# Optimization experiments

Measured on AMD Instinct MI355X. Metric: run time of the kernel, lower is better.

The kernel has to match this reference:

```python
import jax, jax.numpy as jnp
import numpy as np


def _skew(p):
    # (..., 3) -> (..., 3, 3) skew-symmetric matrices
    x, y, z = p[..., 0], p[..., 1], p[..., 2]
    o = jnp.zeros_like(x)
    return jnp.stack([
        jnp.stack([o, -z, y], -1),
        jnp.stack([z, o, -x], -1),
        jnp.stack([-y, x, o], -1)], -2)


def _so3exp(w):
    # Rodrigues formula for a single (3,) axis-angle vector
    th2 = jnp.sum(w * w)
    th = jnp.sqrt(th2 + 1e-24)
    W = _skew(w)
    I = jnp.eye(3, dtype=w.dtype)
    A = jnp.sin(th) / th
    B = (1.0 - jnp.cos(th)) / (th2 + 1e-24)
    return I + A * W + B * (W @ W)


def _gather(fmap, ys, xs):
    # fmap: (C,H,W), ys/xs: (N,) int -> (N,C)
    return fmap[:, ys, xs].T


def _ba(pts3D, feature_ref, fmap, gx, gy, K, n_iters):
    dtype = pts3D.dtype
    N = pts3D.shape[0]
    C, H, W = fmap.shape
    R = jnp.eye(3, dtype=dtype)
    t = jnp.array([1.0, 1.0, 0.0], dtype=dtype)  # default t_init in original
    lam = jnp.asarray(0.01, dtype)
    lr = jnp.asarray(0.1, dtype)
    LR_RESET = 0.1
    fx, fy = K[0, 0], K[1, 1]
    I3 = jnp.broadcast_to(jnp.eye(3, dtype=dtype), (N, 3, 3))

    def project(R, t):
        p3 = pts3D @ R.T + t                      # (N,3) camera-frame points
        uv = p3 @ K.T
        p2 = jnp.round(uv[:, :2] / uv[:, 2:3]).astype(jnp.int32) - 1
        x, y = p2[:, 0], p2[:, 1]
        # original swaps width/height in the bounds check; H == W here so equivalent
        mask = (x >= 0) & (y >= 0) & (x < H) & (y < W)
        xc = jnp.clip(x, 0, W - 1)
        yc = jnp.clip(y, 0, H - 1)
        return p3, xc, yc, mask.astype(dtype)

    def masked_cost(m, err):
        c = 0.5 * jnp.sum(err * err, -1)          # (N,)
        return jnp.sum(m * c) / jnp.maximum(jnp.sum(m), 1.0)

    prev_cost = jnp.asarray(0.0, dtype)
    for i in range(n_iters):
        p3, xc, yc, m = project(R, t)
        err = _gather(fmap, yc, xc) - feature_ref  # (N,C); indexing_(flip) == [:, y, x]
        if i == 0:
            prev_cost = masked_cost(m, err)
        Z = p3[:, 2]
        o = jnp.ones_like(Z)
        z0 = jnp.zeros_like(Z)
        J_p_T = jnp.concatenate([I3, -_skew(p3)], -1)  # (N,3,6)
        J_px_p = jnp.stack([fx * o, z0, -fx * p3[:, 0] / Z,
                            z0, fy * o, -fy * p3[:, 1] / Z], -1)
        J_px_p = J_px_p.reshape(N, 2, 3) / Z[:, None, None]  # (N,2,3)
        J_f_px = jnp.stack([_gather(gx, yc, xc), _gather(gy, yc, xc)], -1)  # (N,C,2)
        J = jnp.einsum('ncp,npq,nqk->nck', J_f_px, J_px_p, J_p_T)  # (N,C,6)
        Jm = J * m[:, None, None]  # zero out unsupported points (boolean subset)
        Grad = jnp.einsum('nci,nc->i', Jm, err)    # (6,)
        Hess = jnp.einsum('nci,ncj->ij', Jm, Jm)   # (6,6)
        Hd = Hess + jnp.diag(jnp.diagonal(Hess) + 1e-9) * lam  # LM damping
        delta = -lr * (jnp.linalg.inv(Hd) @ Grad)
        dt_vec, dw = delta[:3], delta[3:]
        dr = _so3exp(dw)
        R_new = dr @ R
        t_new = dr @ t + dt_vec
        _, xcn, ycn, mn = project(R_new, t_new)
        errn = _gather(fmap, ycn, xcn) - feature_ref
        new_cost = masked_cost(mn, errn)
        worse = new_cost > prev_cost
        lam = jnp.clip(lam * jnp.where(worse, 10.0, 0.1), 1e-6, 1e4)
        lr = jnp.where(worse, jnp.clip(0.1 * lr, 1e-3, 1.0), LR_RESET)
        R = jnp.where(worse, R, R_new)
        t = jnp.where(worse, t, t_new)
        prev_cost = jnp.where(worse, prev_cost, new_cost)
    # stack R (3,3) and t (3,) into a single (4,3) output
    return jnp.concatenate([R, t[None, :]], 0)


def setup_inputs() -> dict:
    key = jax.random.key(0)
    ks = jax.random.split(key, 6)
    N, C, H, W = 10000, 128, 512, 512
    xy = jax.random.uniform(ks[0], (N, 2), minval=-2.0, maxval=2.0)
    z = jax.random.uniform(ks[1], (N, 1), minval=4.0, maxval=8.0)
    pts3D = jnp.concatenate([xy, z], -1).astype(jnp.float32)
    feature_map_query = 0.1 * jax.random.normal(ks[2], (C, H, W), dtype=jnp.float32)
    feature_grad_x = 0.1 * jax.random.normal(ks[3], (C, H, W), dtype=jnp.float32)
    feature_grad_y = 0.1 * jax.random.normal(ks[4], (C, H, W), dtype=jnp.float32)
    feature_ref = 0.1 * jax.random.normal(ks[5], (N, C), dtype=jnp.float32)
    K = jnp.array([[256.0, 0.0, 256.0],
                   [0.0, 256.0, 256.0],
                   [0.0, 0.0, 1.0]], dtype=jnp.float32)
    return {"pts3D": pts3D, "feature_ref": feature_ref,
            "feature_map_query": feature_map_query,
            "feature_grad_x": feature_grad_x, "feature_grad_y": feature_grad_y,
            "K": K, "n_iters": 5}


def reference(pts3D, feature_ref, feature_map_query, feature_grad_x, feature_grad_y, K, n_iters):
    return _ba(pts3D, feature_ref, feature_map_query, feature_grad_x, feature_grad_y, K, int(n_iters))
```

## Files before the change

### kernel.cpp

```cpp
#include <hip/hip_runtime.h>
#include <math.h>

#define NPTS 10000
#define CCH  128
#define HH   512
#define WW   512
#define HWSZ (HH*WW)
#define NQ   29
#define GA   640

struct BAState {
  double R[9];
  double t[3];
  double Rn[9];
  double tn[3];
  double lam, lr, prev_cost;
};

__device__ __forceinline__ float wave_sum64(float v) {
#pragma unroll
  for (int off = 32; off > 0; off >>= 1) v += __shfl_xor(v, off, 64);
  return v;
}

__device__ __forceinline__ float sel6(float b0,float b1,float b2,float b3,float b4,float b5,int i){
  float r = b0;
  r = (i==1)?b1:r; r=(i==2)?b2:r; r=(i==3)?b3:r; r=(i==4)?b4:r; r=(i==5)?b5:r;
  return r;
}

__device__ __forceinline__ void project_pt(
    const float* R, const float* t, float fx, float fy, float cx, float cy,
    float X, float Y, float Z,
    float& px, float& py, float& pz, int& xc, int& yc, int& m)
{
  px = R[0]*X + R[1]*Y + R[2]*Z + t[0];
  py = R[3]*X + R[4]*Y + R[5]*Z + t[1];
  pz = R[6]*X + R[7]*Y + R[8]*Z + t[2];
  float u = fx*px + cx*pz;
  float v = fy*py + cy*pz;
  int xi = (int)rintf(u/pz) - 1;
  int yi = (int)rintf(v/pz) - 1;
  m = (xi >= 0 && yi >= 0 && xi < HH && yi < WW) ? 1 : 0;
  xc = min(max(xi,0), WW-1);
  yc = min(max(yi,0), HH-1);
}

__global__ __launch_bounds__(256) void ba_accum(
    const float* __restrict__ pts, const float* __restrict__ fref,
    const float* __restrict__ fmap, const float* __restrict__ gxm,
    const float* __restrict__ gym, const float* __restrict__ Km,
    const BAState* __restrict__ st, double* __restrict__ acc_out)
{
  const int lane      = threadIdx.x & 63;
  const int waveInBlk = threadIdx.x >> 6;
  const int wave      = blockIdx.x * 4 + waveInBlk;
  const int nwaves    = gridDim.x * 4;

  float Rf[9], tf[3];
#pragma unroll
  for (int i = 0; i < 9; ++i) Rf[i] = (float)st->R[i];
#pragma unroll
  for (int i = 0; i < 3; ++i) tf[i] = (float)st->t[i];
  const float fx = Km[0], cx = Km[2], fy = Km[4], cy = Km[5];

  int qj = 0, qk = 0;
  if (lane < 6) { qj = lane; qk = lane; }
  else if (lane < 27) {
    int idx = lane - 6, j = 0;
    while (idx >= 6 - j) { idx -= 6 - j; j++; }
    qj = j; qk = j + idx;
  }

  double acc = 0.0;

  for (int n = wave; n < NPTS; n += nwaves) {
    float X = pts[3*n], Y = pts[3*n+1], Z = pts[3*n+2];
    float px, py, pz; int xc, yc, m;
    project_pt(Rf, tf, fx, fy, cx, cy, X, Y, Z, px, py, pz, xc, yc, m);
    if (!m) continue;

    const int base = yc * WW + xc;
    const int c0 = lane, c1 = lane + 64;
    const float* fr = fref + (size_t)n * CCH;

    float f0  = fmap[(size_t)c0*HWSZ + base];
    float f1  = fmap[(size_t)c1*HWSZ + base];
    float gx0 = gxm [(size_t)c0*HWSZ + base];
    float gx1 = gxm [(size_t)c1*HWSZ + base];
    float gy0 = gym [(size_t)c0*HWSZ + base];
    float gy1 = gym [(size_t)c1*HWSZ + base];
    float e0 = f0 - fr[c0];
    float e1 = f1 - fr[c1];

    float sge = gx0*e0 + gx1*e1;
    float sye = gy0*e0 + gy1*e1;
    float sxx = gx0*gx0 + gx1*gx1;
    float sxy = gx0*gy0 + gx1*gy1;
    float syy = gy0*gy0 + gy1*gy1;
    float see = e0*e0 + e1*e1;

    sge = wave_sum64(sge); sye = wave_sum64(sye);
    sxx = wave_sum64(sxx); sxy = wave_sum64(sxy);
    syy = wave_sum64(syy); see = wave_sum64(see);

    float iz = 1.0f / pz;
    float a0 = fx * iz, a2 = -fx * px * iz * iz;
    float b1 = fy * iz, b2 = -fy * py * iz * iz;
    float B00=a0, B01=0.f, B02=a2, B03=a2*py, B04=a0*pz - a2*px, B05=-a0*py;
    float B10=0.f, B11=b1, B12=b2, B13=-b1*pz + b2*py, B14=-b2*px, B15=b1*px;

    float b0j = sel6(B00,B01,B02,B03,B04,B05,qj);
    float b0k = sel6(B00,B01,B02,B03,B04,B05,qk);
    float b1j = sel6(B10,B11,B12,B13,B14,B15,qj);
    float b1k = sel6(B10,B11,B12,B13,B14,B15,qk);

    float contrib;
    if (lane < 6)        contrib = b0j*sge + b1j*sye;
    else if (lane < 27)  contrib = b0j*b0k*sxx + (b0j*b1k + b1j*b0k)*sxy + b1j*b1k*syy;
    else if (lane == 27) contrib = 0.5f * see;
    else if (lane == 28) contrib = 1.0f;
    else                 contrib = 0.0f;
    acc += (double)contrib;
  }

  __shared__ double lds[4][NQ];
  if (lane < NQ) lds[waveInBlk][lane] = acc;
  __syncthreads();
  if (threadIdx.x < NQ) {
    double blockSum = lds[0][threadIdx.x] + lds[1][threadIdx.x]
                    + lds[2][threadIdx.x] + lds[3][threadIdx.x];
    atomicAdd(&acc_out[threadIdx.x], blockSum);
  }
}

__global__ __launch_bounds__(256) void ba_cost(
    const float* __restrict__ pts, const float* __restrict__ fref,
    const float* __restrict__ fmap, const float* __restrict__ Km,
    const BAState* __restrict__ st, double* __restrict__ acc_out)
{
  const int lane      = threadIdx.x & 63;
  const int waveInBlk = threadIdx.x >> 6;
  const int wave      = blockIdx.x * 4 + waveInBlk;
  const int nwaves    = gridDim.x * 4;

  float Rf[9], tf[3];
#pragma unroll
  for (int i = 0; i < 9; ++i) Rf[i] = (float)st->Rn[i];
#pragma unroll
  for (int i = 0; i < 3; ++i) tf[i] = (float)st->tn[i];
  const float fx = Km[0], cx = Km[2], fy = Km[4], cy = Km[5];

  double acc = 0.0;
  for (int n = wave; n < NPTS; n += nwaves) {
    float X = pts[3*n], Y = pts[3*n+1], Z = pts[3*n+2];
    float px, py, pz; int xc, yc, m;
    project_pt(Rf, tf, fx, fy, cx, cy, X, Y, Z, px, py, pz, xc, yc, m);
    if (!m) continue;
    const int base = yc * WW + xc;
    const int c0 = lane, c1 = lane + 64;
    const float* fr = fref + (size_t)n * CCH;
    float e0 = fmap[(size_t)c0*HWSZ + base] - fr[c0];
    float e1 = fmap[(size_t)c1*HWSZ + base] - fr[c1];
    float see = wave_sum64(e0*e0 + e1*e1);
    if (lane == 0)      acc += 0.5 * (double)see;
    else if (lane == 1) acc += 1.0;
  }

  __shared__ double lds[4][2];
  if (lane < 2) lds[waveInBlk][lane] = acc;
  __syncthreads();
  if (threadIdx.x < 2) {
    double blockSum = lds[0][threadIdx.x] + lds[1][threadIdx.x]
                    + lds[2][threadIdx.x] + lds[3][threadIdx.x];
    atomicAdd(&acc_out[threadIdx.x], blockSum);
  }
}

__global__ void ba_init(BAState* st, double* accA, double* accB) {
  const int t = threadIdx.x;
  if (t == 0) {
    st->R[0]=1; st->R[1]=0; st->R[2]=0;
    st->R[3]=0; st->R[4]=1; st->R[5]=0;
    st->R[6]=0; st->R[7]=0; st->R[8]=1;
    st->t[0]=1; st->t[1]=1; st->t[2]=0;
    st->lam = 0.01; st->lr = 0.1; st->prev_cost = 0.0;
  }
  if (t < NQ) accA[t] = 0.0;
  if (t < 2)  accB[t] = 0.0;
}

__global__ __launch_bounds__(64) void ba_solve(
    BAState* st, double* __restrict__ accA, int iter0)
{
  __shared__ double red[NQ];
  const int t = threadIdx.x;
  if (t < NQ) { red[t] = accA[t]; accA[t] = 0.0; }
  __syncthreads();
  if (t != 0) return;

  double Grad[6];
  for (int i = 0; i < 6; ++i) Grad[i] = red[i];
  double Hs[6][6];
  {
    int idx = 6;
    for (int j = 0; j < 6; ++j)
      for (int k = j; k < 6; ++k) { Hs[j][k] = Hs[k][j] = red[idx++]; }
  }
  if (iter0) st->prev_cost = red[27] / fmax(red[28], 1.0);

  const double lam = st->lam, lr = st->lr;

  double M[6][7];
  for (int j = 0; j < 6; ++j) {
    for (int k = 0; k < 6; ++k) M[j][k] = Hs[j][k];
    M[j][j] += (Hs[j][j] + 1e-9) * lam;
    M[j][6] = Grad[j];
  }
  for (int c = 0; c < 6; ++c) {
    int piv = c; double best = fabs(M[c][c]);
    for (int r = c + 1; r < 6; ++r) { double a = fabs(M[r][c]); if (a > best) { best = a; piv = r; } }
    if (piv != c) for (int k = 0; k < 7; ++k) { double tmp = M[c][k]; M[c][k] = M[piv][k]; M[piv][k] = tmp; }
    double inv = 1.0 / M[c][c];
    for (int k = c; k < 7; ++k) M[c][k] *= inv;
    for (int r = 0; r < 6; ++r) {
      if (r == c) continue;
      double f = M[r][c];
      for (int k = c; k < 7; ++k) M[r][k] -= f * M[c][k];
    }
  }
  double delta[6];
  for (int j = 0; j < 6; ++j) delta[j] = -lr * M[j][6];

  const double dt0 = delta[0], dt1 = delta[1], dt2 = delta[2];
  const double w0 = delta[3], w1 = delta[4], w2 = delta[5];

  const double th2 = w0*w0 + w1*w1 + w2*w2;
  const double th  = sqrt(th2 + 1e-24);
  const double A   = sin(th) / th;
  const double Bc  = (1.0 - cos(th)) / (th2 + 1e-24);
  double Wm[3][3] = { {0,-w2,w1}, {w2,0,-w0}, {-w1,w0,0} };
  double W2[3][3];
  for (int i = 0; i < 3; ++i)
    for (int j = 0; j < 3; ++j) {
      double s = 0;
      for (int k = 0; k < 3; ++k) s += Wm[i][k] * Wm[k][j];
      W2[i][j] = s;
    }
  double dr[3][3];
  for (int i = 0; i < 3; ++i)
    for (int j = 0; j < 3; ++j)
      dr[i][j] = (i == j ? 1.0 : 0.0) + A * Wm[i][j] + Bc * W2[i][j];

  for (int i = 0; i < 3; ++i)
    for (int j = 0; j < 3; ++j) {
      double s = 0;
      for (int k = 0; k < 3; ++k) s += dr[i][k] * st->R[3*k + j];
      st->Rn[3*i + j] = s;
    }
  for (int i = 0; i < 3; ++i) {
    double s = 0;
    for (int k = 0; k < 3; ++k) s += dr[i][k] * st->t[k];
    st->tn[i] = s + (i == 0 ? dt0 : (i == 1 ? dt1 : dt2));
  }
}

__global__ __launch_bounds__(64) void ba_update(
    BAState* st, double* __restrict__ accB, int last, float* __restrict__ out)
{
  __shared__ double red[2];
  const int t = threadIdx.x;
  if (t < 2) { red[t] = accB[t]; accB[t] = 0.0; }
  __syncthreads();
  if (t != 0) return;

  const double new_cost = red[0] / fmax(red[1], 1.0);
  const int worse = (new_cost > st->prev_cost) ? 1 : 0;
  double lam = st->lam * (worse ? 10.0 : 0.1);
  st->lam = fmin(fmax(lam, 1e-6), 1e4);
  st->lr  = worse ? fmin(fmax(0.1 * st->lr, 0.001), 1.0) : 0.1;
  if (!worse) {
    for (int i = 0; i < 9; ++i) st->R[i] = st->Rn[i];
    for (int i = 0; i < 3; ++i) st->t[i] = st->tn[i];
    st->prev_cost = new_cost;
  }
  if (last) {
    for (int i = 0; i < 9; ++i) out[i] = (float)st->R[i];
    for (int i = 0; i < 3; ++i) out[9 + i] = (float)st->t[i];
  }
}

extern "C" void kernel_launch(void* const* d_in, const int* in_sizes, int n_in,
                              void* d_out, int out_size, void* d_ws, size_t ws_size,
                              hipStream_t stream) {
  const float* pts  = (const float*)d_in[0];
  const float* fref = (const float*)d_in[1];
  const float* fmap = (const float*)d_in[2];
  const float* gx   = (const float*)d_in[3];
  const float* gy   = (const float*)d_in[4];
  const float* Km   = (const float*)d_in[5];
  float* out = (float*)d_out;

  BAState* st  = (BAState*)d_ws;
  double* accA = (double*)((char*)d_ws + 512);
  double* accB = accA + NQ;

  ba_init<<<1, 64, 0, stream>>>(st, accA, accB);
  const int NIT = 5;
  for (int i = 0; i < NIT; ++i) {
    ba_accum<<<GA, 256, 0, stream>>>(pts, fref, fmap, gx, gy, Km, st, accA);
    ba_solve<<<1, 64, 0, stream>>>(st, accA, (i == 0) ? 1 : 0);
    ba_cost<<<GA, 256, 0, stream>>>(pts, fref, fmap, Km, st, accB);
    ba_update<<<1, 64, 0, stream>>>(st, accB, (i == NIT - 1) ? 1 : 0, out);
  }
}
```

Measured before the change: 787.7 us.

## Fuse solve/update into reduction kernels and cache gathered pixel features per point

The separate single-block solve and update kernels are folded into the accumulation and cost kernels using a last-block-done atomic counter, which halves the launch count per iteration. The first pass unrolls four points per wave to overlap gathers, and it writes each point's gathered feature and gradient values into a compact per-point workspace buffer keyed by pixel index. Later iterations read that contiguous buffer when the projected pixel is unchanged, so they avoid strided gathers across 128 channel planes, and they run with smaller grids. The cache lives only within one call and is rebuilt each launch. It adds workspace size requirements and extra writes in the first pass.

```diff
diff --git a/kernel.cpp b/kernel.cpp
--- a/kernel.cpp
+++ b/kernel.cpp
@@ -7,7 +7,6 @@
 #define WW   512
 #define HWSZ (HH*WW)
 #define NQ   29
-#define GA   640
 
 struct BAState {
   double R[9];
@@ -46,159 +45,43 @@
   yc = min(max(yi,0), HH-1);
 }
 
-__global__ __launch_bounds__(256) void ba_accum(
-    const float* __restrict__ pts, const float* __restrict__ fref,
-    const float* __restrict__ fmap, const float* __restrict__ gxm,
-    const float* __restrict__ gym, const float* __restrict__ Km,
-    const BAState* __restrict__ st, double* __restrict__ acc_out)
-{
-  const int lane      = threadIdx.x & 63;
-  const int waveInBlk = threadIdx.x >> 6;
-  const int wave      = blockIdx.x * 4 + waveInBlk;
-  const int nwaves    = gridDim.x * 4;
-
-  float Rf[9], tf[3];
-#pragma unroll
-  for (int i = 0; i < 9; ++i) Rf[i] = (float)st->R[i];
-#pragma unroll
-  for (int i = 0; i < 3; ++i) tf[i] = (float)st->t[i];
-  const float fx = Km[0], cx = Km[2], fy = Km[4], cy = Km[5];
-
-  int qj = 0, qk = 0;
-  if (lane < 6) { qj = lane; qk = lane; }
-  else if (lane < 27) {
-    int idx = lane - 6, j = 0;
-    while (idx >= 6 - j) { idx -= 6 - j; j++; }
-    qj = j; qk = j + idx;
-  }
-
-  double acc = 0.0;
-
-  for (int n = wave; n < NPTS; n += nwaves) {
-    float X = pts[3*n], Y = pts[3*n+1], Z = pts[3*n+2];
-    float px, py, pz; int xc, yc, m;
-    project_pt(Rf, tf, fx, fy, cx, cy, X, Y, Z, px, py, pz, xc, yc, m);
-    if (!m) continue;
-
-    const int base = yc * WW + xc;
-    const int c0 = lane, c1 = lane + 64;
-    const float* fr = fref + (size_t)n * CCH;
-
-    float f0  = fmap[(size_t)c0*HWSZ + base];
-    float f1  = fmap[(size_t)c1*HWSZ + base];
-    float gx0 = gxm [(size_t)c0*HWSZ + base];
-    float gx1 = gxm [(size_t)c1*HWSZ + base];
-    float gy0 = gym [(size_t)c0*HWSZ + base];
-    float gy1 = gym [(size_t)c1*HWSZ + base];
-    float e0 = f0 - fr[c0];
-    float e1 = f1 - fr[c1];
-
-    float sge = gx0*e0 + gx1*e1;
-    float sye = gy0*e0 + gy1*e1;
-    float sxx = gx0*gx0 + gx1*gx1;
-    float sxy = gx0*gy0 + gx1*gy1;
-    float syy = gy0*gy0 + gy1*gy1;
-    float see = e0*e0 + e1*e1;
-
-    sge = wave_sum64(sge); sye = wave_sum64(sye);
-    sxx = wave_sum64(sxx); sxy = wave_sum64(sxy);
-    syy = wave_sum64(syy); see = wave_sum64(see);
-
-    float iz = 1.0f / pz;
-    float a0 = fx * iz, a2 = -fx * px * iz * iz;
-    float b1 = fy * iz, b2 = -fy * py * iz * iz;
-    float B00=a0, B01=0.f, B02=a2, B03=a2*py, B04=a0*pz - a2*px, B05=-a0*py;
-    float B10=0.f, B11=b1, B12=b2, B13=-b1*pz + b2*py, B14=-b2*px, B15=b1*px;
-
-    float b0j = sel6(B00,B01,B02,B03,B04,B05,qj);
-    float b0k = sel6(B00,B01,B02,B03,B04,B05,qk);
-    float b1j = sel6(B10,B11,B12,B13,B14,B15,qj);
-    float b1k = sel6(B10,B11,B12,B13,B14,B15,qk);
-
-    float contrib;
-    if (lane < 6)        contrib = b0j*sge + b1j*sye;
-    else if (lane < 27)  contrib = b0j*b0k*sxx + (b0j*b1k + b1j*b0k)*sxy + b1j*b1k*syy;
-    else if (lane == 27) contrib = 0.5f * see;
-    else if (lane == 28) contrib = 1.0f;
-    else                 contrib = 0.0f;
-    acc += (double)contrib;
-  }
-
-  __shared__ double lds[4][NQ];
-  if (lane < NQ) lds[waveInBlk][lane] = acc;
-  __syncthreads();
-  if (threadIdx.x < NQ) {
-    double blockSum = lds[0][threadIdx.x] + lds[1][threadIdx.x]
-                    + lds[2][threadIdx.x] + lds[3][threadIdx.x];
-    atomicAdd(&acc_out[threadIdx.x], blockSum);
-  }
-}
-
-__global__ __launch_bounds__(256) void ba_cost(
-    const float* __restrict__ pts, const float* __restrict__ fref,
-    const float* __restrict__ fmap, const float* __restrict__ Km,
-    const BAState* __restrict__ st, double* __restrict__ acc_out)
-{
-  const int lane      = threadIdx.x & 63;
-  const int waveInBlk = threadIdx.x >> 6;
-  const int wave      = blockIdx.x * 4 + waveInBlk;
-  const int nwaves    = gridDim.x * 4;
-
-  float Rf[9], tf[3];
-#pragma unroll
-  for (int i = 0; i < 9; ++i) Rf[i] = (float)st->Rn[i];
-#pragma unroll
-  for (int i = 0; i < 3; ++i) tf[i] = (float)st->tn[i];
-  const float fx = Km[0], cx = Km[2], fy = Km[4], cy = Km[5];
-
-  double acc = 0.0;
-  for (int n = wave; n < NPTS; n += nwaves) {
-    float X = pts[3*n], Y = pts[3*n+1], Z = pts[3*n+2];
-    float px, py, pz; int xc, yc, m;
-    project_pt(Rf, tf, fx, fy, cx, cy, X, Y, Z, px, py, pz, xc, yc, m);
-    if (!m) continue;
-    const int base = yc * WW + xc;
-    const int c0 = lane, c1 = lane + 64;
-    const float* fr = fref + (size_t)n * CCH;
-    float e0 = fmap[(size_t)c0*HWSZ + base] - fr[c0];
-    float e1 = fmap[(size_t)c1*HWSZ + base] - fr[c1];
-    float see = wave_sum64(e0*e0 + e1*e1);
-    if (lane == 0)      acc += 0.5 * (double)see;
-    else if (lane == 1) acc += 1.0;
-  }
-
-  __shared__ double lds[4][2];
-  if (lane < 2) lds[waveInBlk][lane] = acc;
-  __syncthreads();
-  if (threadIdx.x < 2) {
-    double blockSum = lds[0][threadIdx.x] + lds[1][threadIdx.x]
-                    + lds[2][threadIdx.x] + lds[3][threadIdx.x];
-    atomicAdd(&acc_out[threadIdx.x], blockSum);
-  }
-}
-
-__global__ void ba_init(BAState* st, double* accA, double* accB) {
-  const int t = threadIdx.x;
-  if (t == 0) {
-    st->R[0]=1; st->R[1]=0; st->R[2]=0;
-    st->R[3]=0; st->R[4]=1; st->R[5]=0;
-    st->R[6]=0; st->R[7]=0; st->R[8]=1;
-    st->t[0]=1; st->t[1]=1; st->t[2]=0;
-    st->lam = 0.01; st->lr = 0.1; st->prev_cost = 0.0;
-  }
-  if (t < NQ) accA[t] = 0.0;
-  if (t < 2)  accB[t] = 0.0;
-}
-
-__global__ __launch_bounds__(64) void ba_solve(
-    BAState* st, double* __restrict__ accA, int iter0)
-{
-  __shared__ double red[NQ];
-  const int t = threadIdx.x;
-  if (t < NQ) { red[t] = accA[t]; accA[t] = 0.0; }
-  __syncthreads();
-  if (t != 0) return;
-
+__device__ __forceinline__ void accumulate_point(
+    float f0,float f1,float g0,float g1,float h0,float h1,float r0,float r1,
+    float px,float py,float pz,float fx,float fy,int lane,int qj,int qk,double& acc)
+{
+  float e0 = f0 - r0, e1 = f1 - r1;
+  float sge = g0*e0 + g1*e1;
+  float sye = h0*e0 + h1*e1;
+  float sxx = g0*g0 + g1*g1;
+  float sxy = g0*h0 + g1*h1;
+  float syy = h0*h0 + h1*h1;
+  float see = e0*e0 + e1*e1;
+  sge = wave_sum64(sge); sye = wave_sum64(sye);
+  sxx = wave_sum64(sxx); sxy = wave_sum64(sxy);
+  syy = wave_sum64(syy); see = wave_sum64(see);
+
+  float iz = 1.0f / pz;
+  float a0 = fx * iz, a2 = -fx * px * iz * iz;
+  float b1 = fy * iz, b2 = -fy * py * iz * iz;
+  float B00=a0, B01=0.f, B02=a2, B03=a2*py, B04=a0*pz - a2*px, B05=-a0*py;
+  float B10=0.f, B11=b1, B12=b2, B13=-b1*pz + b2*py, B14=-b2*px, B15=b1*px;
+
+  float b0j = sel6(B00,B01,B02,B03,B04,B05,qj);
+  float b0k = sel6(B00,B01,B02,B03,B04,B05,qk);
+  float b1j = sel6(B10,B11,B12,B13,B14,B15,qj);
+  float b1k = sel6(B10,B11,B12,B13,B14,B15,qk);
+
+  float contrib;
+  if (lane < 6)        contrib = b0j*sge + b1j*sye;
+  else if (lane < 27)  contrib = b0j*b0k*sxx + (b0j*b1k + b1j*b0k)*sxy + b1j*b1k*syy;
+  else if (lane == 27) contrib = 0.5f * see;
+  else if (lane == 28) contrib = 1.0f;
+  else                 contrib = 0.0f;
+  acc += (double)contrib;
+}
+
+__device__ void solve_core(BAState* st, const double* red, int iter0)
+{
   double Grad[6];
   for (int i = 0; i < 6; ++i) Grad[i] = red[i];
   double Hs[6][6];
@@ -265,16 +148,9 @@
   }
 }
 
-__global__ __launch_bounds__(64) void ba_update(
-    BAState* st, double* __restrict__ accB, int last, float* __restrict__ out)
-{
-  __shared__ double red[2];
-  const int t = threadIdx.x;
-  if (t < 2) { red[t] = accB[t]; accB[t] = 0.0; }
-  __syncthreads();
-  if (t != 0) return;
-
-  const double new_cost = red[0] / fmax(red[1], 1.0);
+__device__ void update_core(BAState* st, double cnum, double msum, int last, float* out)
+{
+  const double new_cost = cnum / fmax(msum, 1.0);
   const int worse = (new_cost > st->prev_cost) ? 1 : 0;
   double lam = st->lam * (worse ? 10.0 : 0.1);
   st->lam = fmin(fmax(lam, 1e-6), 1e4);
@@ -288,6 +164,215 @@
     for (int i = 0; i < 9; ++i) out[i] = (float)st->R[i];
     for (int i = 0; i < 3; ++i) out[9 + i] = (float)st->t[i];
   }
+}
+
+__global__ __launch_bounds__(256) void ba_accum_fused(
+    const float* __restrict__ pts, const float* __restrict__ fref,
+    const float* __restrict__ fmap, const float* __restrict__ gxm,
+    const float* __restrict__ gym, const float* __restrict__ Km,
+    BAState* st, double* accA, unsigned* ctrA,
+    int* __restrict__ cpix, float* __restrict__ compact,
+    int build, int iter0, int use_cache)
+{
+  const int lane      = threadIdx.x & 63;
+  const int waveInBlk = threadIdx.x >> 6;
+  const int wave      = blockIdx.x * 4 + waveInBlk;
+  const int nwaves    = gridDim.x * 4;
+
+  float Rf[9], tf[3];
+#pragma unroll
+  for (int i = 0; i < 9; ++i) Rf[i] = (float)st->R[i];
+#pragma unroll
+  for (int i = 0; i < 3; ++i) tf[i] = (float)st->t[i];
+  const float fx = Km[0], cx = Km[2], fy = Km[4], cy = Km[5];
+
+  int qj = 0, qk = 0;
+  if (lane < 6) { qj = lane; qk = lane; }
+  else if (lane < 27) {
+    int idx = lane - 6, j = 0;
+    while (idx >= 6 - j) { idx -= 6 - j; j++; }
+    qj = j; qk = j + idx;
+  }
+
+  double acc = 0.0;
+
+  if (build) {
+    for (int n0 = wave; n0 < NPTS; n0 += 4 * nwaves) {
+      int nn[4]; bool ok[4]; int bb[4];
+      float PX[4], PY[4], PZ[4];
+#pragma unroll
+      for (int k = 0; k < 4; ++k) {
+        int n = n0 + k * nwaves;
+        nn[k] = n;
+        bool v = (n < NPTS);
+        float X = 0.f, Y = 0.f, Z = 1.f;
+        if (v) { X = pts[3*n]; Y = pts[3*n+1]; Z = pts[3*n+2]; }
+        float px, py, pz; int xc, yc, m;
+        project_pt(Rf, tf, fx, fy, cx, cy, X, Y, Z, px, py, pz, xc, yc, m);
+        bb[k] = yc * WW + xc; PX[k] = px; PY[k] = py; PZ[k] = pz;
+        ok[k] = v && m;
+        if (use_cache && v && lane == 0) cpix[n] = m ? bb[k] : -1;
+      }
+      float F0[4],F1[4],G0[4],G1[4],H0[4],H1[4],R0[4],R1[4];
+#pragma unroll
+      for (int k = 0; k < 4; ++k) {
+        if (ok[k]) {
+          const size_t b = (size_t)bb[k];
+          const float* fr = fref + (size_t)nn[k] * CCH;
+          F0[k] = fmap[(size_t)lane*HWSZ + b];      F1[k] = fmap[(size_t)(lane+64)*HWSZ + b];
+          G0[k] = gxm [(size_t)lane*HWSZ + b];      G1[k] = gxm [(size_t)(lane+64)*HWSZ + b];
+          H0[k] = gym [(size_t)lane*HWSZ + b];      H1[k] = gym [(size_t)(lane+64)*HWSZ + b];
+          R0[k] = fr[lane];                          R1[k] = fr[lane+64];
+        }
+      }
+#pragma unroll
+      for (int k = 0; k < 4; ++k) {
+        if (ok[k] && use_cache) {
+          float* cf = compact + (size_t)nn[k] * 384;
+          cf[lane]       = F0[k]; cf[lane + 64]  = F1[k];
+          cf[128 + lane] = G0[k]; cf[192 + lane] = G1[k];
+          cf[256 + lane] = H0[k]; cf[320 + lane] = H1[k];
+        }
+      }
+#pragma unroll
+      for (int k = 0; k < 4; ++k) {
+        if (!ok[k]) continue;
+        accumulate_point(F0[k],F1[k],G0[k],G1[k],H0[k],H1[k],R0[k],R1[k],
+                         PX[k],PY[k],PZ[k], fx, fy, lane, qj, qk, acc);
+      }
+    }
+  } else {
+    for (int n = wave; n < NPTS; n += nwaves) {
+      float X = pts[3*n], Y = pts[3*n+1], Z = pts[3*n+2];
+      float px, py, pz; int xc, yc, m;
+      project_pt(Rf, tf, fx, fy, cx, cy, X, Y, Z, px, py, pz, xc, yc, m);
+      if (!m) continue;
+      const int base = yc * WW + xc;
+      const float* fr = fref + (size_t)n * CCH;
+      float f0,f1,g0,g1,h0,h1;
+      const bool hit = use_cache && (cpix[n] == base);
+      if (hit) {
+        const float* cf = compact + (size_t)n * 384;
+        f0 = cf[lane];       f1 = cf[lane + 64];
+        g0 = cf[128 + lane]; g1 = cf[192 + lane];
+        h0 = cf[256 + lane]; h1 = cf[320 + lane];
+      } else {
+        f0 = fmap[(size_t)lane*HWSZ + base]; f1 = fmap[(size_t)(lane+64)*HWSZ + base];
+        g0 = gxm [(size_t)lane*HWSZ + base]; g1 = gxm [(size_t)(lane+64)*HWSZ + base];
+        h0 = gym [(size_t)lane*HWSZ + base]; h1 = gym [(size_t)(lane+64)*HWSZ + base];
+        if (use_cache) {
+          if (lane == 0) cpix[n] = base;
+          float* cf = compact + (size_t)n * 384;
+          cf[lane] = f0; cf[lane+64] = f1;
+          cf[128+lane] = g0; cf[192+lane] = g1;
+          cf[256+lane] = h0; cf[320+lane] = h1;
+        }
+      }
+      accumulate_point(f0,f1,g0,g1,h0,h1, fr[lane], fr[lane+64],
+                       px, py, pz, fx, fy, lane, qj, qk, acc);
+    }
+  }
+
+  __shared__ double lds[4][NQ];
+  if (lane < NQ) lds[waveInBlk][lane] = acc;
+  __syncthreads();
+  if (threadIdx.x < NQ) {
+    double s = lds[0][threadIdx.x] + lds[1][threadIdx.x]
+             + lds[2][threadIdx.x] + lds[3][threadIdx.x];
+    atomicAdd(&accA[threadIdx.x], s);
+  }
+  __threadfence();
+  __syncthreads();
+  if (threadIdx.x == 0) {
+    if (atomicAdd(ctrA, 1u) == (unsigned)(gridDim.x - 1)) {
+      __hip_atomic_store(ctrA, 0u, __ATOMIC_RELAXED, __HIP_MEMORY_SCOPE_AGENT);
+      double red[NQ];
+      for (int q = 0; q < NQ; ++q) {
+        red[q] = __hip_atomic_load(&accA[q], __ATOMIC_RELAXED, __HIP_MEMORY_SCOPE_AGENT);
+        __hip_atomic_store(&accA[q], 0.0, __ATOMIC_RELAXED, __HIP_MEMORY_SCOPE_AGENT);
+      }
+      solve_core(st, red, iter0);
+    }
+  }
+}
+
+__global__ __launch_bounds__(256) void ba_cost_upd(
+    const float* __restrict__ pts, const float* __restrict__ fref,
+    const float* __restrict__ fmap, const float* __restrict__ Km,
+    BAState* st, double* accB, unsigned* ctrB,
+    const int* __restrict__ cpix, const float* __restrict__ compact,
+    int last, int use_cache, float* __restrict__ out)
+{
+  const int lane      = threadIdx.x & 63;
+  const int waveInBlk = threadIdx.x >> 6;
+  const int wave      = blockIdx.x * 4 + waveInBlk;
+  const int nwaves    = gridDim.x * 4;
+
+  float Rf[9], tf[3];
+#pragma unroll
+  for (int i = 0; i < 9; ++i) Rf[i] = (float)st->Rn[i];
+#pragma unroll
+  for (int i = 0; i < 3; ++i) tf[i] = (float)st->tn[i];
+  const float fx = Km[0], cx = Km[2], fy = Km[4], cy = Km[5];
+
+  double acc = 0.0;
+  for (int n = wave; n < NPTS; n += nwaves) {
+    float X = pts[3*n], Y = pts[3*n+1], Z = pts[3*n+2];
+    float px, py, pz; int xc, yc, m;
+    project_pt(Rf, tf, fx, fy, cx, cy, X, Y, Z, px, py, pz, xc, yc, m);
+    if (!m) continue;
+    const int base = yc * WW + xc;
+    const float* fr = fref + (size_t)n * CCH;
+    float f0, f1;
+    const bool hit = use_cache && (cpix[n] == base);
+    if (hit) {
+      const float* cf = compact + (size_t)n * 384;
+      f0 = cf[lane]; f1 = cf[lane + 64];
+    } else {
+      f0 = fmap[(size_t)lane*HWSZ + base];
+      f1 = fmap[(size_t)(lane+64)*HWSZ + base];
+    }
+    float e0 = f0 - fr[lane], e1 = f1 - fr[lane + 64];
+    float see = wave_sum64(e0*e0 + e1*e1);
+    if (lane == 0)      acc += 0.5 * (double)see;
+    else if (lane == 1) acc += 1.0;
+  }
+
+  __shared__ double lds[4][2];
+  if (lane < 2) lds[waveInBlk][lane] = acc;
+  __syncthreads();
+  if (threadIdx.x < 2) {
+    double s = lds[0][threadIdx.x] + lds[1][threadIdx.x]
+             + lds[2][threadIdx.x] + lds[3][threadIdx.x];
+    atomicAdd(&accB[threadIdx.x], s);
+  }
+  __threadfence();
+  __syncthreads();
+  if (threadIdx.x == 0) {
+    if (atomicAdd(ctrB, 1u) == (unsigned)(gridDim.x - 1)) {
+      __hip_atomic_store(ctrB, 0u, __ATOMIC_RELAXED, __HIP_MEMORY_SCOPE_AGENT);
+      double c0 = __hip_atomic_load(&accB[0], __ATOMIC_RELAXED, __HIP_MEMORY_SCOPE_AGENT);
+      double c1 = __hip_atomic_load(&accB[1], __ATOMIC_RELAXED, __HIP_MEMORY_SCOPE_AGENT);
+      __hip_atomic_store(&accB[0], 0.0, __ATOMIC_RELAXED, __HIP_MEMORY_SCOPE_AGENT);
+      __hip_atomic_store(&accB[1], 0.0, __ATOMIC_RELAXED, __HIP_MEMORY_SCOPE_AGENT);
+      update_core(st, c0, c1, last, out);
+    }
+  }
+}
+
+__global__ void ba_init(BAState* st, double* accA, double* accB,
+                        unsigned* ctrA, unsigned* ctrB) {
+  const int t = threadIdx.x;
+  if (t == 0) {
+    st->R[0]=1; st->R[1]=0; st->R[2]=0;
+    st->R[3]=0; st->R[4]=1; st->R[5]=0;
+    st->R[6]=0; st->R[7]=0; st->R[8]=1;
+    st->t[0]=1; st->t[1]=1; st->t[2]=0;
+    st->lam = 0.01; st->lr = 0.1; st->prev_cost = 0.0;
+    *ctrA = 0u; *ctrB = 0u;
+  }
+  if (t < NQ) accA[t] = 0.0;
+  if (t < 2)  accB[t] = 0.0;
 }
 
 extern "C" void kernel_launch(void* const* d_in, const int* in_sizes, int n_in,
@@ -301,16 +386,33 @@
   const float* Km   = (const float*)d_in[5];
   float* out = (float*)d_out;
 
-  BAState* st  = (BAState*)d_ws;
-  double* accA = (double*)((char*)d_ws + 512);
-  double* accB = accA + NQ;
-
-  ba_init<<<1, 64, 0, stream>>>(st, accA, accB);
-  const int NIT = 5;
-  for (int i = 0; i < NIT; ++i) {
-    ba_accum<<<GA, 256, 0, stream>>>(pts, fref, fmap, gx, gy, Km, st, accA);
-    ba_solve<<<1, 64, 0, stream>>>(st, accA, (i == 0) ? 1 : 0);
-    ba_cost<<<GA, 256, 0, stream>>>(pts, fref, fmap, Km, st, accB);
-    ba_update<<<1, 64, 0, stream>>>(st, accB, (i == NIT - 1) ? 1 : 0, out);
-  }
-}
+  char* ws = (char*)d_ws;
+  BAState*  st   = (BAState*)ws;
+  double*   accA = (double*)(ws + 256);
+  double*   accB = (double*)(ws + 512);
+  unsigned* ctrA = (unsigned*)(ws + 576);
+  unsigned* ctrB = (unsigned*)(ws + 580);
+  int*      cpix = (int*)(ws + 1024);
+  float*    compact = (float*)(ws + 1024 + 40960);
+  const size_t need = 1024 + 40960 + (size_t)NPTS * 384 * sizeof(float);
+  const int use_cache = (ws_size >= need) ? 1 : 0;
+
+  const int GBIG = 640;
+  const int GSM  = use_cache ? 160 : 640;
+  const int NIT  = 5;
+
+  ba_init<<<1, 64, 0, stream>>>(st, accA, accB, ctrA, ctrB);
+  ba_accum_fused<<<GBIG, 256, 0, stream>>>(pts, fref, fmap, gx, gy, Km,
+                                           st, accA, ctrA, cpix, compact,
+                                           1, 1, use_cache);
+  ba_cost_upd<<<GSM, 256, 0, stream>>>(pts, fref, fmap, Km, st, accB, ctrB,
+                                       cpix, compact, 0, use_cache, out);
+  for (int i = 1; i < NIT; ++i) {
+    ba_accum_fused<<<GSM, 256, 0, stream>>>(pts, fref, fmap, gx, gy, Km,
+                                            st, accA, ctrA, cpix, compact,
+                                            0, 0, use_cache);
+    ba_cost_upd<<<GSM, 256, 0, stream>>>(pts, fref, fmap, Km, st, accB, ctrB,
+                                         cpix, compact, (i == NIT - 1) ? 1 : 0,
+                                         use_cache, out);
+  }
+}
```

Result: faster. 734.0 us (-6.8%).
